# Performance work log

Measured on AMD Instinct MI355X. Metric: run time of the kernel, lower is better.

## Reference

```python
import jax, jax.numpy as jnp
import numpy as np

HEADS = 24
HEAD_DIM = 128
IP_SCALE = 1.0


def _rmsnorm(x, eps, weight=None):
    v = jnp.mean(x * x, axis=-1, keepdims=True)
    y = x * jax.lax.rsqrt(v + eps)
    return y * weight if weight is not None else y


def _rotate_half_interleaved(x):
    # diffusers apply_rotary_emb: pairs (x0, x1) -> (-x1, x0), interleaved
    x2 = x.reshape(*x.shape[:-1], -1, 2)
    rot = jnp.stack([-x2[..., 1], x2[..., 0]], axis=-1)
    return rot.reshape(x.shape)


def _sdpa(q, k, v):
    # q: [B,Sq,H,D], k/v: [B,Sk,H,D]
    scale = 1.0 / jnp.sqrt(jnp.asarray(HEAD_DIM, q.dtype))
    scores = jnp.einsum('bqhd,bkhd->bhqk', q, k) * scale
    p = jax.nn.softmax(scores, axis=-1)
    return jnp.einsum('bhqk,bkhd->bqhd', p, v)


def setup_inputs() -> dict:
    key = jax.random.key(0)
    ks = jax.random.split(key, 10)
    B, S, HID, CAD, T = 1, 2048, 3072, 4096, 128
    sc = 0.02
    return {
        'hidden_states': jax.random.normal(ks[0], (B, S, HID), jnp.float32),
        'cos': jnp.cos(jax.random.normal(ks[1], (S, HEAD_DIM), jnp.float32)),
        'sin': jnp.sin(jax.random.normal(ks[1], (S, HEAD_DIM), jnp.float32)),
        'ip_hidden': jax.random.normal(ks[2], (B, T, CAD), jnp.float32),
        'Wq': jax.random.normal(ks[3], (HID, HID), jnp.float32) * sc,
        'bq': jnp.zeros((HID,), jnp.float32),
        'Wk': jax.random.normal(ks[4], (HID, HID), jnp.float32) * sc,
        'bk': jnp.zeros((HID,), jnp.float32),
        'Wv': jax.random.normal(ks[5], (HID, HID), jnp.float32) * sc,
        'bv': jnp.zeros((HID,), jnp.float32),
        'norm_q_w': jnp.ones((HEAD_DIM,), jnp.float32),
        'norm_k_w': jnp.ones((HEAD_DIM,), jnp.float32),
        'Wk_ip': jax.random.normal(ks[6], (HID, CAD), jnp.float32) * sc,
        'Wv_ip': jax.random.normal(ks[7], (HID, CAD), jnp.float32) * sc,
    }


def reference(hidden_states, cos, sin, ip_hidden, Wq, bq, Wk, bk, Wv, bv,
              norm_q_w, norm_k_w, Wk_ip, Wv_ip):
    B, S, HID = hidden_states.shape
    # QKV projections (FLUX attn has bias=True)
    q = (hidden_states @ Wq.T + bq).reshape(B, S, HEADS, HEAD_DIM)
    k = (hidden_states @ Wk.T + bk).reshape(B, S, HEADS, HEAD_DIM)
    v = (hidden_states @ Wv.T + bv).reshape(B, S, HEADS, HEAD_DIM)
    # QK RMSNorm (affine, eps=1e-6 in FLUX)
    q = _rmsnorm(q, 1e-6, norm_q_w)
    k = _rmsnorm(k, 1e-6, norm_k_w)
    # RoPE (sequence_dim=1): cos/sin [S, D] -> broadcast over batch/heads
    c = cos[None, :, None, :]
    s = sin[None, :, None, :]
    q = q * c + _rotate_half_interleaved(q) * s
    k = k * c + _rotate_half_interleaved(k) * s
    out = _sdpa(q, k, v).reshape(B, S, HID)
    # IP-adapter branch
    T = ip_hidden.shape[1]
    ip_k = (ip_hidden @ Wk_ip.T).reshape(B, T, HEADS, HEAD_DIM)
    ip_v = (ip_hidden @ Wv_ip.T).reshape(B, T, HEADS, HEAD_DIM)
    ip_k = _rmsnorm(ip_k, 1e-5)
    ip_v = _rmsnorm(ip_v, 1e-5)
    ip_attn = _sdpa(q, ip_k, ip_v).reshape(B, S, HID)
    return out + IP_SCALE * ip_attn
```

## Files before the change

kernel.cpp:

```cpp
#include <hip/hip_runtime.h>
#include <stdint.h>

typedef unsigned short u16;
typedef __bf16 bf16x8 __attribute__((ext_vector_type(8)));
typedef float f32x4 __attribute__((ext_vector_type(4)));

#define HEADS 24
#define HD 128
#define S_LEN 2048
#define HID 3072

__device__ __forceinline__ u16 f2bf(float f) {
  union { float f; uint32_t u; } a; a.f = f;
  return (u16)((a.u + 0x7FFFu + ((a.u >> 16) & 1u)) >> 16);
}

__global__ __launch_bounds__(256) void k_f2bf(const float* __restrict__ in,
                                              u16* __restrict__ out, int n4) {
  int i = blockIdx.x * 256 + threadIdx.x;
  if (i >= n4) return;
  float4 v = ((const float4*)in)[i];
  uint2 pk;
  pk.x = (uint32_t)f2bf(v.x) | ((uint32_t)f2bf(v.y) << 16);
  pk.y = (uint32_t)f2bf(v.z) | ((uint32_t)f2bf(v.w) << 16);
  ((uint2*)out)[i] = pk;
}

__global__ __launch_bounds__(256) void k_gemm_bt(
    const u16* __restrict__ A,
    const u16* __restrict__ B0, const u16* __restrict__ B1, const u16* __restrict__ B2,
    const float* __restrict__ bias0, const float* __restrict__ bias1, const float* __restrict__ bias2,
    float* __restrict__ C0, float* __restrict__ C1, float* __restrict__ C2,
    int M, int N, int K)
{
  const int z = blockIdx.z;
  const u16* __restrict__ B = (z == 0) ? B0 : (z == 1 ? B1 : B2);
  const float* __restrict__ bias = (z == 0) ? bias0 : (z == 1 ? bias1 : bias2);
  float* __restrict__ C = (z == 0) ? C0 : (z == 1 ? C1 : C2);
  const int m0 = blockIdx.x * 128, n0 = blockIdx.y * 128;
  const int tid = threadIdx.x, l = tid & 63, w = tid >> 6;
  const int wm = w >> 1, wn = w & 1;
  const int lr = l & 15, lg = l >> 4;

  __shared__ u16 Al[128 * 40];
  __shared__ u16 Bl[128 * 40];

  f32x4 acc[4][4];
#pragma unroll
  for (int m = 0; m < 4; m++)
#pragma unroll
    for (int n = 0; n < 4; n++) acc[m][n] = f32x4{0.f, 0.f, 0.f, 0.f};

  const int sr = tid >> 2;
  const int so = (tid & 3) * 8;
  const u16* Ag  = A + (size_t)(m0 + sr) * K + so;
  const u16* Ag2 = A + (size_t)(m0 + sr + 64) * K + so;
  const u16* Bg  = B + (size_t)(n0 + sr) * K + so;
  const u16* Bg2 = B + (size_t)(n0 + sr + 64) * K + so;
  u16* Aw  = &Al[sr * 40 + so];
  u16* Aw2 = &Al[(sr + 64) * 40 + so];
  u16* Bw  = &Bl[sr * 40 + so];
  u16* Bw2 = &Bl[(sr + 64) * 40 + so];
  const u16* af = &Al[(wm * 64 + lr) * 40 + lg * 8];
  const u16* bp = &Bl[(wn * 64 + lr) * 40 + lg * 8];

  for (int k0 = 0; k0 < K; k0 += 32) {
    if (k0) __syncthreads();
    *(uint4*)Aw  = *(const uint4*)(Ag + k0);
    *(uint4*)Aw2 = *(const uint4*)(Ag2 + k0);
    *(uint4*)Bw  = *(const uint4*)(Bg + k0);
    *(uint4*)Bw2 = *(const uint4*)(Bg2 + k0);
    __syncthreads();
    bf16x8 a[4], b[4];
#pragma unroll
    for (int m = 0; m < 4; m++) a[m] = *(const bf16x8*)(af + m * 16 * 40);
#pragma unroll
    for (int n = 0; n < 4; n++) b[n] = *(const bf16x8*)(bp + n * 16 * 40);
#pragma unroll
    for (int m = 0; m < 4; m++)
#pragma unroll
      for (int n = 0; n < 4; n++)
        acc[m][n] = __builtin_amdgcn_mfma_f32_16x16x32_bf16(a[m], b[n], acc[m][n], 0, 0, 0);
  }

#pragma unroll
  for (int m = 0; m < 4; m++) {
    const int row = m0 + wm * 64 + m * 16 + lg * 4;
#pragma unroll
    for (int n = 0; n < 4; n++) {
      const int col = n0 + wn * 64 + n * 16 + lr;
      const float bs = bias[col];
#pragma unroll
      for (int r = 0; r < 4; r++)
        C[(size_t)(row + r) * N + col] = acc[m][n][r] + bs;
    }
  }
}

__global__ __launch_bounds__(256) void k_norm_rope(
    const float* __restrict__ Qraw, const float* __restrict__ Kraw,
    const float* __restrict__ cosp, const float* __restrict__ sinp,
    const float* __restrict__ wq, const float* __restrict__ wk,
    u16* __restrict__ Qh, u16* __restrict__ Kh)
{
  const int isK = blockIdx.y;
  const float* __restrict__ src = isK ? Kraw : Qraw;
  const float* __restrict__ wgt = isK ? wk : wq;
  u16* __restrict__ dst = isK ? Kh : Qh;
  const float scl = isK ? 1.0f : 0.08838834764831845f;
  const int w4 = threadIdx.x >> 6, l = threadIdx.x & 63;
  const int row = blockIdx.x * 4 + w4;
  const int s = row / 24, h = row - s * 24;
  const float2 x = *(const float2*)&src[(size_t)s * HID + h * HD + 2 * l];
  float ss = x.x * x.x + x.y * x.y;
#pragma unroll
  for (int off = 32; off; off >>= 1) ss += __shfl_xor(ss, off);
  const float rn = rsqrtf(ss * (1.0f / 128.0f) + 1e-6f);
  const float w0 = wgt[2 * l], w1 = wgt[2 * l + 1];
  const float c0 = cosp[s * HD + 2 * l], c1 = cosp[s * HD + 2 * l + 1];
  const float s0 = sinp[s * HD + 2 * l], s1 = sinp[s * HD + 2 * l + 1];
  const float y0 = x.x * rn * w0, y1 = x.y * rn * w1;
  const float o0 = (y0 * c0 - y1 * s0) * scl;
  const float o1 = (y1 * c1 + y0 * s1) * scl;
  const uint32_t pk = (uint32_t)f2bf(o0) | ((uint32_t)f2bf(o1) << 16);
  *(uint32_t*)&dst[((size_t)h * S_LEN + s) * HD + 2 * l] = pk;
}

__global__ __launch_bounds__(256) void k_ip_norm(
    const float* __restrict__ Kraw, const float* __restrict__ Vraw,
    u16* __restrict__ Kh, float* __restrict__ Vn)
{
  const int isV = blockIdx.y;
  const float* __restrict__ src = isV ? Vraw : Kraw;
  const int w4 = threadIdx.x >> 6, l = threadIdx.x & 63;
  const int row = blockIdx.x * 4 + w4;
  const int t = row / 24, h = row - t * 24;
  const float2 x = *(const float2*)&src[(size_t)t * HID + h * HD + 2 * l];
  float ss = x.x * x.x + x.y * x.y;
#pragma unroll
  for (int off = 32; off; off >>= 1) ss += __shfl_xor(ss, off);
  const float rn = rsqrtf(ss * (1.0f / 128.0f) + 1e-5f);
  const float o0 = x.x * rn, o1 = x.y * rn;
  if (isV) {
    *(float2*)&Vn[(size_t)t * HID + h * HD + 2 * l] = make_float2(o0, o1);
  } else {
    const uint32_t pk = (uint32_t)f2bf(o0) | ((uint32_t)f2bf(o1) << 16);
    *(uint32_t*)&Kh[((size_t)h * 128 + t) * HD + 2 * l] = pk;
  }
}

__global__ __launch_bounds__(256) void k_transpose(
    const float* __restrict__ X, u16* __restrict__ Y, int S)
{
  const int h = blockIdx.z, d0 = blockIdx.y * 32, s0 = blockIdx.x * 32;
  __shared__ float tile[32][33];
  const int c = threadIdx.x & 31, rb = threadIdx.x >> 5;
#pragma unroll
  for (int i = 0; i < 4; i++) {
    const int r = rb + i * 8;
    tile[r][c] = X[(size_t)(s0 + r) * HID + h * HD + d0 + c];
  }
  __syncthreads();
#pragma unroll
  for (int i = 0; i < 4; i++) {
    const int r = rb + i * 8;
    Y[((size_t)h * HD + d0 + r) * S + s0 + c] = f2bf(tile[c][r]);
  }
}

__global__ __launch_bounds__(256) void k_attn(
    const u16* __restrict__ Q, const u16* __restrict__ K, const u16* __restrict__ Vt,
    float* __restrict__ Out, int kv_len, int add)
{
  const int h = blockIdx.y;
  const int q0 = blockIdx.x * 64;
  const int tid = threadIdx.x, w = tid >> 6, l = tid & 63;
  const int lr = l & 15, lg = l >> 4;

  __shared__ u16 Kl[64][136];
  __shared__ u16 Vl[128][88];
  __shared__ u16 Pl[4][16][88];

  bf16x8 qf[4];
  {
    const u16* qp = &Q[((size_t)h * S_LEN + q0 + w * 16 + lr) * HD];
#pragma unroll
    for (int db = 0; db < 4; db++) qf[db] = *(const bf16x8*)&qp[db * 32 + lg * 8];
  }

  float m_[4], ls[4];
  f32x4 acc[8];
#pragma unroll
  for (int r = 0; r < 4; r++) { m_[r] = -1e30f; ls[r] = 0.f; }
#pragma unroll
  for (int nb = 0; nb < 8; nb++) acc[nb] = f32x4{0.f, 0.f, 0.f, 0.f};

  for (int kv0 = 0; kv0 < kv_len; kv0 += 64) {
#pragma unroll
    for (int i = 0; i < 4; i++) {
      const int c = tid + i * 256;
      { const int r = c >> 4, o = (c & 15) * 8;
        *(uint4*)&Kl[r][o] = *(const uint4*)&K[((size_t)h * kv_len + kv0 + r) * HD + o]; }
      { const int r = c >> 3, o = (c & 7) * 8;
        *(uint4*)&Vl[r][o] = *(const uint4*)&Vt[((size_t)h * HD + r) * kv_len + kv0 + o]; }
    }
    __syncthreads();

    f32x4 sf[4];
#pragma unroll
    for (int kb = 0; kb < 4; kb++) {
      f32x4 s = f32x4{0.f, 0.f, 0.f, 0.f};
#pragma unroll
      for (int db = 0; db < 4; db++) {
        bf16x8 b = *(const bf16x8*)&Kl[kb * 16 + lr][db * 32 + lg * 8];
        s = __builtin_amdgcn_mfma_f32_16x16x32_bf16(qf[db], b, s, 0, 0, 0);
      }
      sf[kb] = s;
    }

    float pv[4][4], rescv[4];
#pragma unroll
    for (int r = 0; r < 4; r++) {
      float tm = fmaxf(fmaxf(sf[0][r], sf[1][r]), fmaxf(sf[2][r], sf[3][r]));
#pragma unroll
      for (int off = 8; off; off >>= 1) tm = fmaxf(tm, __shfl_xor(tm, off));
      const float mn = fmaxf(m_[r], tm);
      const float resc = __expf(m_[r] - mn);
      float ps = 0.f;
#pragma unroll
      for (int kb = 0; kb < 4; kb++) { const float p = __expf(sf[kb][r] - mn); pv[kb][r] = p; ps += p; }
#pragma unroll
      for (int off = 8; off; off >>= 1) ps += __shfl_xor(ps, off);
      ls[r] = ls[r] * resc + ps;
      m_[r] = mn; rescv[r] = resc;
    }
#pragma unroll
    for (int nb = 0; nb < 8; nb++)
#pragma unroll
      for (int r = 0; r < 4; r++) acc[nb][r] *= rescv[r];

#pragma unroll
    for (int kb = 0; kb < 4; kb++)
#pragma unroll
      for (int r = 0; r < 4; r++)
        Pl[w][lg * 4 + r][kb * 16 + lr] = f2bf(pv[kb][r]);

    __syncthreads();

#pragma unroll
    for (int kb = 0; kb < 2; kb++) {
      bf16x8 a = *(const bf16x8*)&Pl[w][lr][kb * 32 + lg * 8];
#pragma unroll
      for (int nb = 0; nb < 8; nb++) {
        bf16x8 b = *(const bf16x8*)&Vl[nb * 16 + lr][kb * 32 + lg * 8];
        acc[nb] = __builtin_amdgcn_mfma_f32_16x16x32_bf16(a, b, acc[nb], 0, 0, 0);
      }
    }
    __syncthreads();
  }

  float inv[4];
#pragma unroll
  for (int r = 0; r < 4; r++) inv[r] = 1.0f / ls[r];
#pragma unroll
  for (int nb = 0; nb < 8; nb++)
#pragma unroll
    for (int r = 0; r < 4; r++) {
      const int row = q0 + w * 16 + lg * 4 + r;
      const int col = h * HD + nb * 16 + lr;
      const size_t idx = (size_t)row * HID + col;
      const float v = acc[nb][r] * inv[r];
      if (add) Out[idx] += v; else Out[idx] = v;
    }
}

extern "C" void kernel_launch(void* const* d_in, const int* in_sizes, int n_in,
                              void* d_out, int out_size, void* d_ws, size_t ws_size,
                              hipStream_t stream) {
  const float* hs   = (const float*)d_in[0];
  const float* cosp = (const float*)d_in[1];
  const float* sinp = (const float*)d_in[2];
  const float* iph  = (const float*)d_in[3];
  const float* Wq   = (const float*)d_in[4];
  const float* bq   = (const float*)d_in[5];
  const float* Wk   = (const float*)d_in[6];
  const float* bk   = (const float*)d_in[7];
  const float* Wv   = (const float*)d_in[8];
  const float* bv   = (const float*)d_in[9];
  const float* nqw  = (const float*)d_in[10];
  const float* nkw  = (const float*)d_in[11];
  const float* Wkip = (const float*)d_in[12];
  const float* Wvip = (const float*)d_in[13];
  float* out = (float*)d_out;

  uint8_t* base = (uint8_t*)d_ws;
  size_t off = 0;
  auto alloc = [&](size_t bytes) { uint8_t* p = base + off; off += (bytes + 255) & ~(size_t)255; return p; };

  u16* X16 = (u16*)alloc(2048ull * 3072 * 2);
  uint8_t* regionB = base + off;
  u16* W16q  = (u16*)alloc(3072ull * 3072 * 2);
  u16* W16k  = (u16*)alloc(3072ull * 3072 * 2);
  u16* W16v  = (u16*)alloc(3072ull * 3072 * 2);
  u16* Wip16k = (u16*)alloc(3072ull * 4096 * 2);
  u16* Wip16v = (u16*)alloc(3072ull * 4096 * 2);
  u16* ip16   = (u16*)alloc(128ull * 4096 * 2);
  float* Qraw = (float*)alloc(2048ull * 3072 * 4);
  float* Kraw = (float*)alloc(2048ull * 3072 * 4);
  float* Vraw = (float*)alloc(2048ull * 3072 * 4);
  float* ipKraw = (float*)alloc(128ull * 3072 * 4);
  float* ipVraw = (float*)alloc(128ull * 3072 * 4);

  uint8_t* dp = regionB;
  auto allocD = [&](size_t bytes) { uint8_t* p = dp; dp += (bytes + 255) & ~(size_t)255; return p; };
  u16* Qh   = (u16*)allocD(24ull * 2048 * 128 * 2);
  u16* Kh   = (u16*)allocD(24ull * 2048 * 128 * 2);
  u16* Vt   = (u16*)allocD(24ull * 128 * 2048 * 2);
  u16* ipKh = (u16*)allocD(24ull * 128 * 128 * 2);
  u16* ipVt = (u16*)allocD(24ull * 128 * 128 * 2);
  float* ipVn = (float*)allocD(128ull * 3072 * 4);

  k_f2bf<<<6144, 256, 0, stream>>>(hs, X16, 1572864);
  k_f2bf<<<9216, 256, 0, stream>>>(Wq, W16q, 2359296);
  k_f2bf<<<9216, 256, 0, stream>>>(Wk, W16k, 2359296);
  k_f2bf<<<9216, 256, 0, stream>>>(Wv, W16v, 2359296);
  k_f2bf<<<12288, 256, 0, stream>>>(Wkip, Wip16k, 3145728);
  k_f2bf<<<12288, 256, 0, stream>>>(Wvip, Wip16v, 3145728);
  k_f2bf<<<512, 256, 0, stream>>>(iph, ip16, 131072);

  k_gemm_bt<<<dim3(16, 24, 3), 256, 0, stream>>>(X16, W16q, W16k, W16v, bq, bk, bv,
                                                 Qraw, Kraw, Vraw, 2048, 3072, 3072);
  k_gemm_bt<<<dim3(1, 24, 2), 256, 0, stream>>>(ip16, Wip16k, Wip16v, Wip16v, bq, bq, bq,
                                                ipKraw, ipVraw, ipVraw, 128, 3072, 4096);

  k_norm_rope<<<dim3(12288, 2), 256, 0, stream>>>(Qraw, Kraw, cosp, sinp, nqw, nkw, Qh, Kh);
  k_ip_norm<<<dim3(768, 2), 256, 0, stream>>>(ipKraw, ipVraw, ipKh, ipVn);
  k_transpose<<<dim3(64, 4, 24), 256, 0, stream>>>(Vraw, Vt, 2048);
  k_transpose<<<dim3(4, 4, 24), 256, 0, stream>>>(ipVn, ipVt, 128);

  k_attn<<<dim3(32, 24), 256, 0, stream>>>(Qh, Kh, Vt, out, 2048, 0);
  k_attn<<<dim3(32, 24), 256, 0, stream>>>(Qh, ipKh, ipVt, out, 128, 1);
}
```

Measured before the change: 726.7 us.

## Use direct global-to-LDS loads in GEMM and split-K the IP projection

The GEMM now stages A and B tiles with global_load_lds builtins straight into unpadded LDS, instead of going through registers into padded shared arrays. The small IP-adapter projection is split along K into four chunks that accumulate with atomicAdd into zeroed outputs, which raises its block count from 48 to 192. The attention kernel also drops a __syncthreads between writing P to LDS and reading it back. Risks: the unpadded layout may cause LDS bank conflicts, atomics make the summation order nondeterministic, and removing the barrier relies on each wave only reading its own P rows.

```diff
diff --git a/kernel.cpp b/kernel.cpp
--- a/kernel.cpp
+++ b/kernel.cpp
@@ -13,6 +13,12 @@
 __device__ __forceinline__ u16 f2bf(float f) {
   union { float f; uint32_t u; } a; a.f = f;
   return (u16)((a.u + 0x7FFFu + ((a.u >> 16) & 1u)) >> 16);
+}
+
+__device__ __forceinline__ void gload16(const u16* g, u16* lds) {
+  __builtin_amdgcn_global_load_lds(
+      (const __attribute__((address_space(1))) void*)g,
+      (__attribute__((address_space(3))) void*)lds, 16, 0, 0);
 }
 
 __global__ __launch_bounds__(256) void k_f2bf(const float* __restrict__ in,
@@ -31,19 +37,22 @@
     const u16* __restrict__ B0, const u16* __restrict__ B1, const u16* __restrict__ B2,
     const float* __restrict__ bias0, const float* __restrict__ bias1, const float* __restrict__ bias2,
     float* __restrict__ C0, float* __restrict__ C1, float* __restrict__ C2,
-    int M, int N, int K)
+    int N, int K, int atomic_split)
 {
   const int z = blockIdx.z;
   const u16* __restrict__ B = (z == 0) ? B0 : (z == 1 ? B1 : B2);
   const float* __restrict__ bias = (z == 0) ? bias0 : (z == 1 ? bias1 : bias2);
   float* __restrict__ C = (z == 0) ? C0 : (z == 1 ? C1 : C2);
-  const int m0 = blockIdx.x * 128, n0 = blockIdx.y * 128;
+  const int m0 = atomic_split ? 0 : blockIdx.x * 128;
+  const int n0 = blockIdx.y * 128;
+  const int kb = atomic_split ? blockIdx.x * atomic_split : 0;
+  const int ke = atomic_split ? kb + atomic_split : K;
   const int tid = threadIdx.x, l = tid & 63, w = tid >> 6;
   const int wm = w >> 1, wn = w & 1;
   const int lr = l & 15, lg = l >> 4;
 
-  __shared__ u16 Al[128 * 40];
-  __shared__ u16 Bl[128 * 40];
+  __shared__ u16 Al[128 * 32];
+  __shared__ u16 Bl[128 * 32];
 
   f32x4 acc[4][4];
 #pragma unroll
@@ -51,31 +60,26 @@
 #pragma unroll
     for (int n = 0; n < 4; n++) acc[m][n] = f32x4{0.f, 0.f, 0.f, 0.f};
 
-  const int sr = tid >> 2;
-  const int so = (tid & 3) * 8;
-  const u16* Ag  = A + (size_t)(m0 + sr) * K + so;
-  const u16* Ag2 = A + (size_t)(m0 + sr + 64) * K + so;
-  const u16* Bg  = B + (size_t)(n0 + sr) * K + so;
-  const u16* Bg2 = B + (size_t)(n0 + sr + 64) * K + so;
-  u16* Aw  = &Al[sr * 40 + so];
-  u16* Aw2 = &Al[(sr + 64) * 40 + so];
-  u16* Bw  = &Bl[sr * 40 + so];
-  u16* Bw2 = &Bl[(sr + 64) * 40 + so];
-  const u16* af = &Al[(wm * 64 + lr) * 40 + lg * 8];
-  const u16* bp = &Bl[(wn * 64 + lr) * 40 + lg * 8];
-
-  for (int k0 = 0; k0 < K; k0 += 32) {
-    if (k0) __syncthreads();
-    *(uint4*)Aw  = *(const uint4*)(Ag + k0);
-    *(uint4*)Aw2 = *(const uint4*)(Ag2 + k0);
-    *(uint4*)Bw  = *(const uint4*)(Bg + k0);
-    *(uint4*)Bw2 = *(const uint4*)(Bg2 + k0);
+  const int srow = l >> 2, scol = (l & 3) * 8;
+  const u16* Ab = A + (size_t)(m0 + srow) * K + scol;
+  const u16* Bb = B + (size_t)(n0 + srow) * K + scol;
+  const u16* af = &Al[(wm * 64 + lr) * 32 + lg * 8];
+  const u16* bf = &Bl[(wn * 64 + lr) * 32 + lg * 8];
+
+  for (int k0 = kb; k0 < ke; k0 += 32) {
+    if (k0 != kb) __syncthreads();
+#pragma unroll
+    for (int j = 0; j < 2; j++) {
+      const int c = j * 4 + w;
+      gload16(Ab + (size_t)c * 16 * K + k0, &Al[c * 512]);
+      gload16(Bb + (size_t)c * 16 * K + k0, &Bl[c * 512]);
+    }
     __syncthreads();
     bf16x8 a[4], b[4];
 #pragma unroll
-    for (int m = 0; m < 4; m++) a[m] = *(const bf16x8*)(af + m * 16 * 40);
-#pragma unroll
-    for (int n = 0; n < 4; n++) b[n] = *(const bf16x8*)(bp + n * 16 * 40);
+    for (int m = 0; m < 4; m++) a[m] = *(const bf16x8*)(af + m * 16 * 32);
+#pragma unroll
+    for (int n = 0; n < 4; n++) b[n] = *(const bf16x8*)(bf + n * 16 * 32);
 #pragma unroll
     for (int m = 0; m < 4; m++)
 #pragma unroll
@@ -83,16 +87,30 @@
         acc[m][n] = __builtin_amdgcn_mfma_f32_16x16x32_bf16(a[m], b[n], acc[m][n], 0, 0, 0);
   }
 
-#pragma unroll
-  for (int m = 0; m < 4; m++) {
-    const int row = m0 + wm * 64 + m * 16 + lg * 4;
-#pragma unroll
-    for (int n = 0; n < 4; n++) {
-      const int col = n0 + wn * 64 + n * 16 + lr;
-      const float bs = bias[col];
-#pragma unroll
-      for (int r = 0; r < 4; r++)
-        C[(size_t)(row + r) * N + col] = acc[m][n][r] + bs;
+  if (atomic_split) {
+#pragma unroll
+    for (int m = 0; m < 4; m++) {
+      const int row = m0 + wm * 64 + m * 16 + lg * 4;
+#pragma unroll
+      for (int n = 0; n < 4; n++) {
+        const int col = n0 + wn * 64 + n * 16 + lr;
+#pragma unroll
+        for (int r = 0; r < 4; r++)
+          atomicAdd(&C[(size_t)(row + r) * N + col], acc[m][n][r]);
+      }
+    }
+  } else {
+#pragma unroll
+    for (int m = 0; m < 4; m++) {
+      const int row = m0 + wm * 64 + m * 16 + lg * 4;
+#pragma unroll
+      for (int n = 0; n < 4; n++) {
+        const int col = n0 + wn * 64 + n * 16 + lr;
+        const float bs = bias[col];
+#pragma unroll
+        for (int r = 0; r < 4; r++)
+          C[(size_t)(row + r) * N + col] = acc[m][n][r] + bs;
+      }
     }
   }
 }
@@ -245,7 +263,6 @@
       for (int r = 0; r < 4; r++)
         Pl[w][lg * 4 + r][kb * 16 + lr] = f2bf(pv[kb][r]);
 
-    __syncthreads();
 
 #pragma unroll
     for (int kb = 0; kb < 2; kb++) {
@@ -328,10 +345,13 @@
   k_f2bf<<<12288, 256, 0, stream>>>(Wvip, Wip16v, 3145728);
   k_f2bf<<<512, 256, 0, stream>>>(iph, ip16, 131072);
 
+  hipMemsetAsync(ipKraw, 0, 128ull * 3072 * 4, stream);
+  hipMemsetAsync(ipVraw, 0, 128ull * 3072 * 4, stream);
+
   k_gemm_bt<<<dim3(16, 24, 3), 256, 0, stream>>>(X16, W16q, W16k, W16v, bq, bk, bv,
-                                                 Qraw, Kraw, Vraw, 2048, 3072, 3072);
-  k_gemm_bt<<<dim3(1, 24, 2), 256, 0, stream>>>(ip16, Wip16k, Wip16v, Wip16v, bq, bq, bq,
-                                                ipKraw, ipVraw, ipVraw, 128, 3072, 4096);
+                                                 Qraw, Kraw, Vraw, 3072, 3072, 0);
+  k_gemm_bt<<<dim3(4, 24, 2), 256, 0, stream>>>(ip16, Wip16k, Wip16v, Wip16v, bq, bq, bq,
+                                                ipKraw, ipVraw, ipVraw, 3072, 4096, 1024);
 
   k_norm_rope<<<dim3(12288, 2), 256, 0, stream>>>(Qraw, Kraw, cosp, sinp, nqw, nkw, Qh, Kh);
   k_ip_norm<<<dim3(768, 2), 256, 0, stream>>>(ipKraw, ipVraw, ipKh, ipVn);
```

Result: faster. 687.2 us (-5.4%).
